# Performance work log

Measured on AMD Instinct MI355X. Metric: run time of the kernel, lower is better.

Reference implementation:

```python
import jax, jax.numpy as jnp
import numpy as np

NUM_OBJ = 3
MIN_OBJ_SCALE = 0.1
MAX_OBJ_SCALE = 0.8
MIN_Y_SCALE = 0.75
MAX_Y_SCALE = 1.25
OBJ_POS_BOUND = 0.9
EPS_FIX = 0.095
BIG = 1e12


def setup_inputs() -> dict:
    key = jax.random.key(0)
    k1, k2, k3 = jax.random.split(key, 3)
    n, T, C, H, W = 64, 32, 3, 64, 64
    x = jax.random.normal(k1, (n, T, C, H, W), dtype=jnp.float32)
    d = C * H * W
    W_enc = jax.random.normal(k2, (d, NUM_OBJ * 8), dtype=jnp.float32) / np.sqrt(d).astype(np.float32)
    b_enc = jax.random.normal(k3, (NUM_OBJ * 8,), dtype=jnp.float32) * 0.01
    return {"x": x, "W_enc": W_enc, "b_enc": b_enc}


def _constrain_zp_mean(zp):
    # zp: (nTo, 8) -> mean (nTo, 4). std branch is discarded by forward().
    zm = jnp.concatenate([jax.nn.sigmoid(zp[:, 0:2]), 2.0 * jax.nn.sigmoid(zp[:, 2:4]) - 1.0], -1)
    set_max = jnp.array([[MAX_OBJ_SCALE - MIN_OBJ_SCALE, MAX_Y_SCALE - MIN_Y_SCALE, OBJ_POS_BOUND, OBJ_POS_BOUND]], dtype=zp.dtype)
    set_min = jnp.array([[MIN_OBJ_SCALE, MIN_Y_SCALE, 0.0, 0.0]], dtype=zp.dtype)
    return zm * set_max + set_min


def _greedy_assign(errors):
    # errors: (n, o, o). Greedy row-by-row argmin, masking out used columns with BIG,
    # exactly as the torch fault-fix loop does via scatter of 1e12.
    n, o, _ = errors.shape
    def step(used, i):
        e = errors[:, i, :] + used * BIG
        j = jnp.argmin(e, -1)
        used = used + jax.nn.one_hot(j, o, dtype=errors.dtype)
        return used, j
    _, js = jax.lax.scan(step, jnp.zeros((n, o), errors.dtype), jnp.arange(o))
    return jnp.moveaxis(js, 0, 1)  # (n, o)


def _match_objects(z):
    # z: (n, T, o, 4). Sequential greedy matching over time.
    def step(prev, z_t):
        curr = jax.lax.stop_gradient(z_t[:, :, 2:4])          # (n, o, 2)
        prv = jax.lax.stop_gradient(prev[:, :, 2:4])          # (n, o, 2)
        errors = jnp.sum((prv[:, :, None, :] - curr[:, None, :, :]) ** 2, -1)  # (n, i, j)
        idx = jnp.argmin(errors, -1)                          # (n, o)
        # fault = assignment is not a permutation (num_obj==3 check from source)
        ok = jnp.all(idx[:, 1:] != idx[:, :-1], -1) & (idx[:, 0] != idx[:, 2])
        gidx = _greedy_assign(errors)
        idx = jnp.where(ok[:, None], idx, gidx)
        match = jnp.take_along_axis(z_t, idx[:, :, None], axis=1)
        return match, match
    z0 = z[:, 0]
    _, rest = jax.lax.scan(step, z0, jnp.moveaxis(z[:, 1:], 1, 0))
    return jnp.concatenate([z0[:, None], jnp.moveaxis(rest, 0, 1)], 1)


def _fix_supair(z):
    # z: (n, T, o, 4). Replace isolated position jumps with neighbor average.
    n, T, o, d = z.shape
    diffs = jax.lax.stop_gradient(jnp.abs(z[:, 1:, :, :2] - z[:, :-1, :, :2]))
    zpad2 = jnp.zeros((n, 1, o, 2), z.dtype)
    prev = jnp.concatenate([zpad2, diffs], 1)
    after = jnp.concatenate([diffs, zpad2], 1)
    mask = (prev > EPS_FIX) & (after > EPS_FIX)               # (n, T, o, 2)
    zpad = jnp.zeros((n, 1, o, d), z.dtype)
    smooth = jnp.concatenate([zpad, (z[:, :-2] + z[:, 2:]) / 2, zpad], 1)
    mask_full = jnp.concatenate((d // 2) * [mask], -1)        # (n, T, o, 4)
    return jnp.where(mask_full, smooth, z)


def reference(x, W_enc, b_enc):
    n, T = x.shape[0], x.shape[1]
    # encoder: per-frame linear to (num_obj, 8) z-parameters
    zp = x.reshape(n * T, -1) @ W_enc + b_enc                  # (nT, o*8)
    zm = _constrain_zp_mean(zp.reshape(-1, 8))                 # (nTo, 4)
    z = zm.reshape(n, T, NUM_OBJ, 4)
    z = _match_objects(z)
    z = _fix_supair(z)
    # v_from_state
    v = z[:, 1:, :, 2:] - z[:, :-1, :, 2:]
    zf = jnp.concatenate([z[:, 1:], v], -1)                    # (n, T-1, o, 6)
    zf = jnp.concatenate([jnp.zeros_like(zf[:, 0:1]), zf], 1)  # (n, T, o, 6)
    zf = zf[:, 1:, :, 2:]                                      # (n, T-1, o, 4)
    zf = jnp.concatenate([(zf[..., :2] + 1) / 2 * 10, zf[..., 2:] / 2 * 10], -1)
    zf = jnp.concatenate([zf[..., :2] / 5, zf[..., 2:] * 2], -1)
    return zf
```

## Files before the change

### kernel.cpp

```cpp
#include <hip/hip_runtime.h>

#define N_B   64
#define T_S   32
#define DIM   12288
#define ROWS  2048
#define NCOL  12
#define RPB   4
#define TILE  1024
#define NTILE (DIM / TILE)

__global__ __launch_bounds__(256) void k_tw(const float* __restrict__ W,
                                            float* __restrict__ Wt) {
    const int idx = blockIdx.x * 256 + threadIdx.x;
    const int c   = idx / DIM;
    const int k   = idx - c * DIM;
    const int cm  = ((c >> 2) << 3) | (c & 3);
    Wt[idx] = W[k * 24 + cm];
}

__global__ __launch_bounds__(256, 2) void k_gemm(const float* __restrict__ x,
                                                 const float* __restrict__ Wt,
                                                 const float* __restrict__ b_enc,
                                                 float* __restrict__ zbuf) {
    const int r0  = blockIdx.x * RPB;
    const int tid = threadIdx.x;

    float acc[RPB][NCOL];
#pragma unroll
    for (int r = 0; r < RPB; ++r)
#pragma unroll
        for (int c = 0; c < NCOL; ++c) acc[r][c] = 0.f;

#pragma unroll 2
    for (int t = 0; t < NTILE; ++t) {
        const int kb = t * TILE + tid * 4;
        float4 wv[NCOL];
#pragma unroll
        for (int c = 0; c < NCOL; ++c)
            wv[c] = *(const float4*)(Wt + (size_t)c * DIM + kb);
        float4 xv[RPB];
#pragma unroll
        for (int r = 0; r < RPB; ++r)
            xv[r] = *(const float4*)(x + (size_t)(r0 + r) * DIM + kb);
#pragma unroll
        for (int r = 0; r < RPB; ++r)
#pragma unroll
            for (int c = 0; c < NCOL; ++c)
                acc[r][c] += xv[r].x * wv[c].x + xv[r].y * wv[c].y +
                             xv[r].z * wv[c].z + xv[r].w * wv[c].w;
    }

#pragma unroll
    for (int r = 0; r < RPB; ++r)
#pragma unroll
        for (int c = 0; c < NCOL; ++c) {
            float v = acc[r][c];
            v += __shfl_xor(v, 32, 64);
            v += __shfl_xor(v, 16, 64);
            v += __shfl_xor(v, 8, 64);
            v += __shfl_xor(v, 4, 64);
            v += __shfl_xor(v, 2, 64);
            v += __shfl_xor(v, 1, 64);
            acc[r][c] = v;
        }

    __shared__ float red[4][RPB * NCOL];
    const int wave = tid >> 6;
    const int lane = tid & 63;
    if (lane == 0) {
#pragma unroll
        for (int r = 0; r < RPB; ++r)
#pragma unroll
            for (int c = 0; c < NCOL; ++c)
                red[wave][r * NCOL + c] = acc[r][c];
    }
    __syncthreads();

    if (tid < RPB * NCOL) {
        float s = red[0][tid] + red[1][tid] + red[2][tid] + red[3][tid];
        const int r  = tid / NCOL;
        const int c  = tid - r * NCOL;
        const int o  = c >> 2;
        const int cp = c & 3;
        s += b_enc[o * 8 + cp];
        const float sg = 1.f / (1.f + expf(-s));
        float v;
        if (cp == 0)      v = sg * 0.7f + 0.1f;
        else if (cp == 1) v = sg * 0.5f + 0.75f;
        else              v = (2.f * sg - 1.f) * 0.9f;
        zbuf[(size_t)(r0 + r) * NCOL + c] = v;
    }
}

__global__ __launch_bounds__(64) void k_post(const float* __restrict__ zbuf,
                                             float* __restrict__ out) {
    __shared__ float z[T_S * NCOL];
    __shared__ float zm[T_S * NCOL];
    __shared__ float zf[T_S * NCOL];
    __shared__ int   perm[T_S];
    const int b   = blockIdx.x;
    const int tid = threadIdx.x;

#pragma unroll
    for (int i = 0; i < 6; ++i)
        z[tid + 64 * i] = zbuf[b * 384 + tid + 64 * i];
    __syncthreads();

    if (tid == 0) {
        float px0 = z[2],  py0 = z[3];
        float px1 = z[6],  py1 = z[7];
        float px2 = z[10], py2 = z[11];
        for (int t = 1; t < T_S; ++t) {
            const int base = t * 12;
            const float cx0 = z[base + 2],  cy0 = z[base + 3];
            const float cx1 = z[base + 6],  cy1 = z[base + 7];
            const float cx2 = z[base + 10], cy2 = z[base + 11];

            float dx, dy;
            dx = px0 - cx0; dy = py0 - cy0; const float e00 = dx * dx + dy * dy;
            dx = px0 - cx1; dy = py0 - cy1; const float e01 = dx * dx + dy * dy;
            dx = px0 - cx2; dy = py0 - cy2; const float e02 = dx * dx + dy * dy;
            dx = px1 - cx0; dy = py1 - cy0; const float e10 = dx * dx + dy * dy;
            dx = px1 - cx1; dy = py1 - cy1; const float e11 = dx * dx + dy * dy;
            dx = px1 - cx2; dy = py1 - cy2; const float e12 = dx * dx + dy * dy;
            dx = px2 - cx0; dy = py2 - cy0; const float e20 = dx * dx + dy * dy;
            dx = px2 - cx1; dy = py2 - cy1; const float e21 = dx * dx + dy * dy;
            dx = px2 - cx2; dy = py2 - cy2; const float e22 = dx * dx + dy * dy;

            auto amin3 = [](float a0, float a1, float a2) {
                int j = 0; float e = a0;
                if (a1 < e) { e = a1; j = 1; }
                if (a2 < e) { j = 2; }
                return j;
            };
            int i0 = amin3(e00, e01, e02);
            int i1 = amin3(e10, e11, e12);
            int i2 = amin3(e20, e21, e22);
            const bool ok = (i1 != i0) && (i2 != i1) && (i0 != i2);
            if (!ok) {
                float u0 = 0.f, u1 = 0.f, u2 = 0.f;
                i0 = amin3(e00, e01, e02);
                if (i0 == 0) u0 = 1.f; else if (i0 == 1) u1 = 1.f; else u2 = 1.f;
                i1 = amin3(e10 + u0 * 1e12f, e11 + u1 * 1e12f, e12 + u2 * 1e12f);
                if (i1 == 0) u0 = 1.f; else if (i1 == 1) u1 = 1.f; else u2 = 1.f;
                i2 = amin3(e20 + u0 * 1e12f, e21 + u1 * 1e12f, e22 + u2 * 1e12f);
            }
            perm[t] = i0 * 9 + i1 * 3 + i2;
            px0 = (i0 == 0) ? cx0 : (i0 == 1) ? cx1 : cx2;
            py0 = (i0 == 0) ? cy0 : (i0 == 1) ? cy1 : cy2;
            px1 = (i1 == 0) ? cx0 : (i1 == 1) ? cx1 : cx2;
            py1 = (i1 == 0) ? cy0 : (i1 == 1) ? cy1 : cy2;
            px2 = (i2 == 0) ? cx0 : (i2 == 1) ? cx1 : cx2;
            py2 = (i2 == 0) ? cy0 : (i2 == 1) ? cy1 : cy2;
        }
    }
    __syncthreads();

#pragma unroll
    for (int ii = 0; ii < 6; ++ii) {
        const int i  = tid + 64 * ii;
        const int t  = i / 12;
        const int j  = i - t * 12;
        const int k  = j >> 2;
        const int ch = j & 3;
        int p = k;
        if (t > 0) {
            const int code = perm[t];
            p = (k == 0) ? code / 9 : (k == 1) ? (code % 9) / 3 : code % 3;
        }
        zm[i] = z[t * 12 + p * 4 + ch];
    }
    __syncthreads();

#pragma unroll
    for (int ii = 0; ii < 6; ++ii) {
        const int i  = tid + 64 * ii;
        const int t  = i / 12;
        const int j  = i - t * 12;
        const int o  = j >> 2;
        const int cc = j & 1;
        const int mb = o * 4 + cc;
        const float pd = (t >= 1)  ? fabsf(zm[t * 12 + mb] - zm[(t - 1) * 12 + mb]) : 0.f;
        const float ad = (t <= 30) ? fabsf(zm[(t + 1) * 12 + mb] - zm[t * 12 + mb]) : 0.f;
        const bool  m  = (pd > 0.095f) && (ad > 0.095f);
        const float sm = (t >= 1 && t <= 30)
                             ? (zm[(t - 1) * 12 + j] + zm[(t + 1) * 12 + j]) * 0.5f
                             : 0.f;
        zf[i] = m ? sm : zm[t * 12 + j];
    }
    __syncthreads();

    for (int i = tid; i < 31 * 12; i += 64) {
        const int t  = i / 12;
        const int j  = i - t * 12;
        const int o  = j >> 2;
        const int c2 = j & 3;
        const int pb = o * 4 + 2 + (c2 & 1);
        float v;
        if (c2 < 2) v = zf[(t + 1) * 12 + pb] + 1.f;
        else        v = (zf[(t + 1) * 12 + pb] - zf[t * 12 + pb]) * 10.f;
        out[b * 372 + i] = v;
    }
}

extern "C" void kernel_launch(void* const* d_in, const int* in_sizes, int n_in,
                              void* d_out, int out_size, void* d_ws, size_t ws_size,
                              hipStream_t stream) {
    (void)in_sizes; (void)n_in; (void)out_size; (void)ws_size;
    const float* x     = (const float*)d_in[0];
    const float* W_enc = (const float*)d_in[1];
    const float* b_enc = (const float*)d_in[2];
    float* out  = (float*)d_out;

    float* zbuf = (float*)d_ws;
    float* Wt   = zbuf + ROWS * NCOL;

    k_tw  <<<(NCOL * DIM) / 256, 256, 0, stream>>>(W_enc, Wt);
    k_gemm<<<ROWS / RPB, 256, 0, stream>>>(x, Wt, b_enc, zbuf);
    k_post<<<N_B, 64, 0, stream>>>(zbuf, out);
}
```

Before: 175.8 us.

## Split GEMM reduction dimension across blocks with separate reduce kernel

```diff
diff --git a/kernel.cpp b/kernel.cpp
--- a/kernel.cpp
+++ b/kernel.cpp
@@ -6,8 +6,12 @@
 #define ROWS  2048
 #define NCOL  12
 #define RPB   4
+#define KSPL  4
+#define KSEG  (DIM / KSPL)
 #define TILE  1024
-#define NTILE (DIM / TILE)
+#define NTILE (KSEG / TILE)
+
+typedef float f4 __attribute__((ext_vector_type(4)));
 
 __global__ __launch_bounds__(256) void k_tw(const float* __restrict__ W,
                                             float* __restrict__ Wt) {
@@ -18,11 +22,13 @@
     Wt[idx] = W[k * 24 + cm];
 }
 
-__global__ __launch_bounds__(256, 2) void k_gemm(const float* __restrict__ x,
-                                                 const float* __restrict__ Wt,
-                                                 const float* __restrict__ b_enc,
-                                                 float* __restrict__ zbuf) {
-    const int r0  = blockIdx.x * RPB;
+__global__ __launch_bounds__(256) void k_gemm(const float* __restrict__ x,
+                                              const float* __restrict__ Wt,
+                                              float* __restrict__ part) {
+    const int rb  = blockIdx.x >> 2;
+    const int sg  = blockIdx.x & 3;
+    const int r0  = rb * RPB;
+    const int k00 = sg * KSEG;
     const int tid = threadIdx.x;
 
     float acc[RPB][NCOL];
@@ -31,23 +37,24 @@
 #pragma unroll
         for (int c = 0; c < NCOL; ++c) acc[r][c] = 0.f;
 
-#pragma unroll 2
+#pragma unroll
     for (int t = 0; t < NTILE; ++t) {
-        const int kb = t * TILE + tid * 4;
-        float4 wv[NCOL];
+        const int kb = k00 + t * TILE + tid * 4;
+        f4 wv[NCOL];
 #pragma unroll
         for (int c = 0; c < NCOL; ++c)
-            wv[c] = *(const float4*)(Wt + (size_t)c * DIM + kb);
-        float4 xv[RPB];
+            wv[c] = *(const f4*)(Wt + (size_t)c * DIM + kb);
+        f4 xv[RPB];
 #pragma unroll
         for (int r = 0; r < RPB; ++r)
-            xv[r] = *(const float4*)(x + (size_t)(r0 + r) * DIM + kb);
+            xv[r] = __builtin_nontemporal_load(
+                        (const f4*)(x + (size_t)(r0 + r) * DIM + kb));
 #pragma unroll
         for (int r = 0; r < RPB; ++r)
 #pragma unroll
             for (int c = 0; c < NCOL; ++c)
-                acc[r][c] += xv[r].x * wv[c].x + xv[r].y * wv[c].y +
-                             xv[r].z * wv[c].z + xv[r].w * wv[c].w;
+                acc[r][c] += xv[r][0] * wv[c][0] + xv[r][1] * wv[c][1] +
+                             xv[r][2] * wv[c][2] + xv[r][3] * wv[c][3];
     }
 
 #pragma unroll
@@ -77,19 +84,28 @@
     __syncthreads();
 
     if (tid < RPB * NCOL) {
-        float s = red[0][tid] + red[1][tid] + red[2][tid] + red[3][tid];
-        const int r  = tid / NCOL;
-        const int c  = tid - r * NCOL;
-        const int o  = c >> 2;
-        const int cp = c & 3;
-        s += b_enc[o * 8 + cp];
-        const float sg = 1.f / (1.f + expf(-s));
-        float v;
-        if (cp == 0)      v = sg * 0.7f + 0.1f;
-        else if (cp == 1) v = sg * 0.5f + 0.75f;
-        else              v = (2.f * sg - 1.f) * 0.9f;
-        zbuf[(size_t)(r0 + r) * NCOL + c] = v;
-    }
+        const float s = red[0][tid] + red[1][tid] + red[2][tid] + red[3][tid];
+        part[(size_t)sg * (ROWS * NCOL) + (size_t)r0 * NCOL + tid] = s;
+    }
+}
+
+__global__ __launch_bounds__(256) void k_reduce(const float* __restrict__ part,
+                                                const float* __restrict__ b_enc,
+                                                float* __restrict__ zbuf) {
+    const int rc = blockIdx.x * 256 + threadIdx.x;
+    float s = part[rc] + part[ROWS * NCOL + rc] +
+              part[2 * ROWS * NCOL + rc] + part[3 * ROWS * NCOL + rc];
+
+    const int c  = rc % NCOL;
+    const int o  = c >> 2;
+    const int cp = c & 3;
+    s += b_enc[o * 8 + cp];
+    const float sg = 1.f / (1.f + expf(-s));
+    float v;
+    if (cp == 0)      v = sg * 0.7f + 0.1f;
+    else if (cp == 1) v = sg * 0.5f + 0.75f;
+    else              v = (2.f * sg - 1.f) * 0.9f;
+    zbuf[rc] = v;
 }
 
 __global__ __launch_bounds__(64) void k_post(const float* __restrict__ zbuf,
@@ -214,8 +230,10 @@
 
     float* zbuf = (float*)d_ws;
     float* Wt   = zbuf + ROWS * NCOL;
-
-    k_tw  <<<(NCOL * DIM) / 256, 256, 0, stream>>>(W_enc, Wt);
-    k_gemm<<<ROWS / RPB, 256, 0, stream>>>(x, Wt, b_enc, zbuf);
-    k_post<<<N_B, 64, 0, stream>>>(zbuf, out);
-}
+    float* part = Wt + NCOL * DIM;
+
+    k_tw    <<<(NCOL * DIM) / 256, 256, 0, stream>>>(W_enc, Wt);
+    k_gemm  <<<(ROWS / RPB) * KSPL, 256, 0, stream>>>(x, Wt, part);
+    k_reduce<<<(ROWS * NCOL) / 256, 256, 0, stream>>>(part, b_enc, zbuf);
+    k_post  <<<N_B, 64, 0, stream>>>(zbuf, out);
+}
```

New measurement: 180.0 us. 2.4% more time.
